# Optimization experiments

Hardware: AMD Instinct MI355X
Metric: run time of the kernel (lower is better)

## Reference

```python
import jax, jax.numpy as jnp
import numpy as np

# Fixed multi-scale geometry implied by the module's hard-coded reshapes
# (48^2=2304, 24^2=576, 12^2=144; Len_q = 576).
SPATIAL = [(48, 48), (24, 24), (12, 12)]
NH, NP, NL = 6, 4, 3  # num_heads, num_points, num_levels


def _process_reference_points(rp):
    """rp: (B, 3024, 2) normalized refs over 3 levels -> (B, 576, 2).
    Mirrors the part1/part2/part3 averaging in MSDeformAttn.forward."""
    B = rp.shape[0]
    p1 = rp[:, :2304].reshape(B, 48, 48, 2).mean(axis=(1, 2))[:, None, :]
    p1 = jnp.broadcast_to(p1, (B, 576, 2))
    p2 = rp[:, 2304:2880].reshape(B, 576, 2)
    p3 = rp[:, 2880:].reshape(B, 12, 12, 2)
    p3 = jax.image.resize(p3, (B, 24, 24, 2), 'bilinear')  # align_corners=False
    p3 = p3.reshape(B, 576, 2)
    return (p1 + p2 + p3) / 3.0


def _bilinear_sample(val_l, coords, Hl, Wl):
    """val_l: (B, Hl*Wl, nh, d) one level's values.
    coords: (B, Lq, nh, P, 2) normalized (x, y) sampling locations.
    Returns (B, Lq, P, nh, d) bilinearly sampled values (zero padding)."""
    B, Lq, nh, P, _ = coords.shape
    px = coords[..., 0] * Wl - 0.5
    py = coords[..., 1] * Hl - 0.5
    x0 = jnp.floor(px)
    y0 = jnp.floor(py)
    lx = px - x0
    ly = py - y0
    x0i = x0.astype(jnp.int32)
    y0i = y0.astype(jnp.int32)

    def _flat(a):  # (B,Lq,nh,P) -> (B,Lq*P,nh,1) matching value layout
        return a.transpose(0, 1, 3, 2).reshape(B, Lq * P, nh, 1)

    def gather(xi, yi):
        valid = (xi >= 0) & (xi < Wl) & (yi >= 0) & (yi < Hl)
        xi_c = jnp.clip(xi, 0, Wl - 1)
        yi_c = jnp.clip(yi, 0, Hl - 1)
        idx = _flat(yi_c * Wl + xi_c)
        v = jnp.take_along_axis(val_l, idx, axis=1)  # (B,Lq*P,nh,d)
        return v * _flat(valid).astype(val_l.dtype)

    w00 = _flat((1 - lx) * (1 - ly))
    w10 = _flat(lx * (1 - ly))
    w01 = _flat((1 - lx) * ly)
    w11 = _flat(lx * ly)
    out = (gather(x0i, y0i) * w00 + gather(x0i + 1, y0i) * w10 +
           gather(x0i, y0i + 1) * w01 + gather(x0i + 1, y0i + 1) * w11)
    return out.reshape(B, Lq, P, nh, -1)


def setup_inputs() -> dict:
    key = jax.random.key(0)
    ks = jax.random.split(key, 8)
    B, C = 32, 384
    Lq, Lv = 576, 3024
    # reference points exactly as get_reference_points builds them
    refs = []
    for (Hl, Wl) in SPATIAL:
        ry, rx = np.meshgrid(np.linspace(0.5, Hl - 0.5, Hl) / Hl,
                             np.linspace(0.5, Wl - 0.5, Wl) / Wl, indexing='ij')
        refs.append(np.stack([rx.ravel(), ry.ravel()], -1))
    rp = np.concatenate(refs, 0).astype(np.float32)  # (3024, 2)
    rp = np.broadcast_to(rp[None, :, None, :], (B, Lv, 1, 2)).copy()
    s = 1.0 / np.sqrt(C)
    return {
        'query': jax.random.normal(ks[0], (B, Lq, C), jnp.float32),
        'value': jax.random.normal(ks[1], (B, Lv, C), jnp.float32),
        'reference_points': jnp.asarray(rp),
        'W_value': jax.random.normal(ks[2], (C, C), jnp.float32) * s,
        'b_value': jnp.zeros((C,), jnp.float32),
        'W_off': jax.random.normal(ks[3], (C, NH * NL * NP * 2), jnp.float32) * 0.01,
        'b_off': jnp.zeros((NH * NL * NP * 2,), jnp.float32),
        'W_attn': jax.random.normal(ks[4], (C, NH * NL * NP), jnp.float32) * s,
        'b_attn': jnp.zeros((NH * NL * NP,), jnp.float32),
        'W_out': jax.random.normal(ks[5], (C, C), jnp.float32) * s,
        'b_out': jnp.zeros((C,), jnp.float32),
    }


def reference(query, value, reference_points, W_value, b_value, W_off, b_off,
              W_attn, b_attn, W_out, b_out):
    B, Lq, C = query.shape
    d = C // NH
    val = (value @ W_value + b_value).reshape(B, -1, NH, d)
    off = (query @ W_off + b_off).reshape(B, Lq, NH, NL, NP, 2)
    attn = jax.nn.softmax((query @ W_attn + b_attn)
                          .reshape(B, Lq, NH, NL * NP), axis=-1)
    attn = attn.reshape(B, Lq, NH, NL, NP)
    ref = _process_reference_points(reference_points.reshape(B, -1, 2))
    coords = off + ref[:, :, None, None, None, :]  # (B,Lq,nh,L,P,2)
    out = jnp.zeros((B, Lq, NH, d), query.dtype)
    start = 0
    for l, (Hl, Wl) in enumerate(SPATIAL):
        val_l = val[:, start:start + Hl * Wl]
        sampled = _bilinear_sample(val_l, coords[:, :, :, l], Hl, Wl)
        out = out + jnp.einsum('bqpnd,bqnp->bqnd', sampled, attn[:, :, :, l])
        start += Hl * Wl
    return out.reshape(B, Lq, NH * d) @ W_out + b_out
```

## Files before the change

kernel.cpp:

```cpp
#include <hip/hip_runtime.h>
#include <cmath>

#define B_SZ   32
#define LQ     576
#define LV     3024
#define CDIM   384
#define NHEAD  6
#define DHEAD  64
#define NLVL   3
#define NPTS   4
#define NPROJ  216
#define NPROJP 256

typedef short    bx4 __attribute__((ext_vector_type(4)));
typedef short    bx8 __attribute__((ext_vector_type(8)));
typedef float    fx4 __attribute__((ext_vector_type(4)));
typedef _Float16 hx8 __attribute__((ext_vector_type(8)));

__device__ __forceinline__ short f2bf(float f) {
    unsigned u = __builtin_bit_cast(unsigned, f);
    unsigned r = (u + 0x7FFFu + ((u >> 16) & 1u)) >> 16;
    return (short)r;
}
__device__ __forceinline__ float bf2f(unsigned short u) {
    return __builtin_bit_cast(float, ((unsigned)u) << 16);
}
__device__ __forceinline__ short f2h(float f) {
    return __builtin_bit_cast(short, (_Float16)f);
}

__global__ __launch_bounds__(256) void cast_bf16_kernel(
    const float4* __restrict__ in, bx8* __restrict__ outv, int n8)
{
    const int i = blockIdx.x * 256 + threadIdx.x;
    if (i >= n8) return;
    const float4 a = in[2 * i], b = in[2 * i + 1];
    bx8 s;
    s[0] = f2bf(a.x); s[1] = f2bf(a.y); s[2] = f2bf(a.z); s[3] = f2bf(a.w);
    s[4] = f2bf(b.x); s[5] = f2bf(b.y); s[6] = f2bf(b.z); s[7] = f2bf(b.w);
    outv[i] = s;
}

__global__ __launch_bounds__(256) void cast_transpose_kernel(
    const float* __restrict__ W, short* __restrict__ Wt, int K, int N)
{
    int idx = blockIdx.x * 256 + threadIdx.x;
    if (idx >= K * N) return;
    int n = idx / K, k = idx - n * K;
    Wt[idx] = f2bf(W[(size_t)k * N + n]);
}

__global__ __launch_bounds__(256) void prep_proj_f16_kernel(
    const float* __restrict__ W_off, const float* __restrict__ b_off,
    const float* __restrict__ W_attn, const float* __restrict__ b_attn,
    short* __restrict__ Wf, float* __restrict__ bc)
{
    int idx = blockIdx.x * 256 + threadIdx.x;
    if (idx >= NPROJP * CDIM) return;
    int n = idx / CDIM, k = idx - n * CDIM;
    float w = 0.f;
    if (n < 144)           w = W_off[(size_t)k * 144 + n];
    else if (n < NPROJ)    w = W_attn[(size_t)k * 72 + (n - 144)];
    Wf[idx] = f2h(w);
    if (idx < NPROJP)
        bc[idx] = (idx < 144) ? b_off[idx]
                 : (idx < NPROJ ? b_attn[idx - 144] : 0.f);
}

template <bool OUT_BF16>
__global__ __launch_bounds__(256) void gemm_dma_kernel(
    const short* __restrict__ A, const short* __restrict__ Bt,
    const float* __restrict__ bias, void* __restrict__ Cout,
    int M, int K)
{
    constexpr int N = 384;
    __shared__ short As[128 * 64];
    __shared__ short Bs[128 * 64];

    const int tid = threadIdx.x;
    const int n0 = blockIdx.x * 128;
    const int m0 = blockIdx.y * 128;

    const int w  = tid >> 6;
    const int l  = tid & 63;
    const int wr = (w & 1) * 64;
    const int wc = (w >> 1) * 64;
    const int lr = l & 15;
    const int q  = l >> 4;

    const int rg  = l >> 3;
    const int cg  = l & 7;
    const int csw = cg ^ rg;

    fx4 acc[4][4] = {};

    for (int k0 = 0; k0 < K; k0 += 64) {
        #pragma unroll
        for (int t = 0; t < 4; ++t) {
            const int rbase = w * 32 + t * 8;
            const short* gA = A + (size_t)(m0 + rbase + rg) * K + k0 + csw * 8;
            __builtin_amdgcn_global_load_lds(
                (const __attribute__((address_space(1))) void*)gA,
                (__attribute__((address_space(3))) void*)&As[rbase * 64],
                16, 0, 0);
            const short* gB = Bt + (size_t)(n0 + rbase + rg) * K + k0 + csw * 8;
            __builtin_amdgcn_global_load_lds(
                (const __attribute__((address_space(1))) void*)gB,
                (__attribute__((address_space(3))) void*)&Bs[rbase * 64],
                16, 0, 0);
        }
        __syncthreads();

        #pragma unroll
        for (int ks = 0; ks < 2; ++ks) {
            bx8 af[4], bf[4];
            #pragma unroll
            for (int i = 0; i < 4; ++i)
                af[i] = *(const bx8*)&As[(wr + i * 16 + lr) * 64 +
                                         (((ks * 4 + q) ^ (lr & 7)) << 3)];
            #pragma unroll
            for (int j = 0; j < 4; ++j)
                bf[j] = *(const bx8*)&Bs[(wc + j * 16 + lr) * 64 +
                                         (((ks * 4 + q) ^ (lr & 7)) << 3)];
            #pragma unroll
            for (int i = 0; i < 4; ++i)
                #pragma unroll
                for (int j = 0; j < 4; ++j)
                    acc[i][j] = __builtin_amdgcn_mfma_f32_16x16x32_bf16(
                        af[i], bf[j], acc[i][j], 0, 0, 0);
        }
        __syncthreads();
    }

    const int rrow = q * 4;
    #pragma unroll
    for (int j = 0; j < 4; ++j) {
        const int col = n0 + wc + j * 16 + lr;
        const float bv = bias[col];
        #pragma unroll
        for (int i = 0; i < 4; ++i) {
            const int row = m0 + wr + i * 16 + rrow;
            #pragma unroll
            for (int r = 0; r < 4; ++r) {
                if (OUT_BF16)
                    ((short*)Cout)[(size_t)(row + r) * N + col] = f2bf(acc[i][j][r] + bv);
                else
                    ((float*)Cout)[(size_t)(row + r) * N + col] = acc[i][j][r] + bv;
            }
        }
    }
}

__global__ __launch_bounds__(256) void gemm_proj_kernel(
    const float* __restrict__ A, const short* __restrict__ Wf,
    const float* __restrict__ bias, float* __restrict__ C,
    int M, int K)
{
    __shared__ short As[128 * 72];
    __shared__ short Bs[128 * 72];

    const int tid = threadIdx.x;
    const int n0 = blockIdx.x * 128;
    const int m0 = blockIdx.y * 128;

    const int w  = tid >> 6;
    const int l  = tid & 63;
    const int wr = (w & 1) * 64;
    const int wc = (w >> 1) * 64;
    const int lr = l & 15;
    const int ko = (l >> 4) * 8;

    fx4 acc[4][4] = {};

    for (int k0 = 0; k0 < K; k0 += 64) {
        #pragma unroll
        for (int r = 0; r < 8; ++r) {
            const int id = tid + r * 256;
            const int m  = id >> 4;
            const int kq = (id & 15) << 2;
            const float4 v = *(const float4*)(A + (size_t)(m0 + m) * K + k0 + kq);
            bx4 s;
            s[0] = f2h(v.x); s[1] = f2h(v.y); s[2] = f2h(v.z); s[3] = f2h(v.w);
            *(bx4*)&As[m * 72 + kq] = s;
        }
        #pragma unroll
        for (int r = 0; r < 4; ++r) {
            const int id = tid + r * 256;
            const int n  = id >> 3;
            const int k8 = (id & 7) << 3;
            *(bx8*)&Bs[n * 72 + k8] = *(const bx8*)(Wf + (size_t)(n0 + n) * K + k0 + k8);
        }
        __syncthreads();

        #pragma unroll
        for (int ks = 0; ks < 2; ++ks) {
            bx8 af[4], bf[4];
            #pragma unroll
            for (int i = 0; i < 4; ++i)
                af[i] = *(const bx8*)&As[(wr + i * 16 + lr) * 72 + ks * 32 + ko];
            #pragma unroll
            for (int j = 0; j < 4; ++j)
                bf[j] = *(const bx8*)&Bs[(wc + j * 16 + lr) * 72 + ks * 32 + ko];
            #pragma unroll
            for (int i = 0; i < 4; ++i)
                #pragma unroll
                for (int j = 0; j < 4; ++j)
                    acc[i][j] = __builtin_amdgcn_mfma_f32_16x16x32_f16(
                        __builtin_bit_cast(hx8, af[i]),
                        __builtin_bit_cast(hx8, bf[j]), acc[i][j], 0, 0, 0);
        }
        __syncthreads();
    }

    const int rrow = (l >> 4) * 4;
    #pragma unroll
    for (int j = 0; j < 4; ++j) {
        const int col = n0 + wc + j * 16 + lr;
        if (col >= NPROJ) continue;
        const float bv = bias[col];
        #pragma unroll
        for (int i = 0; i < 4; ++i) {
            const int row = m0 + wr + i * 16 + rrow;
            #pragma unroll
            for (int r = 0; r < 4; ++r)
                C[(size_t)(row + r) * NPROJ + col] = acc[i][j][r] + bv;
        }
    }
}

__global__ __launch_bounds__(256) void ref_kernel(
    const float* __restrict__ rp, float* __restrict__ refp)
{
    const int b = blockIdx.x;
    const float* r = rp + (size_t)b * LV * 2;
    const int tid = threadIdx.x;

    __shared__ float redx[256], redy[256];
    float sx = 0.f, sy = 0.f;
    for (int i = tid; i < 2304; i += 256) {
        sx += r[2 * i + 0];
        sy += r[2 * i + 1];
    }
    redx[tid] = sx; redy[tid] = sy;
    __syncthreads();
    for (int s = 128; s > 0; s >>= 1) {
        if (tid < s) { redx[tid] += redx[tid + s]; redy[tid] += redy[tid + s]; }
        __syncthreads();
    }
    const float p1x = redx[0] * (1.f / 2304.f);
    const float p1y = redy[0] * (1.f / 2304.f);

    const float* g = r + 2880 * 2;
    for (int q = tid; q < 576; q += 256) {
        const float p2x = r[(2304 + q) * 2 + 0];
        const float p2y = r[(2304 + q) * 2 + 1];
        const int qy = q / 24, qx = q % 24;
        const float syc = fminf(fmaxf(0.5f * qy - 0.25f, 0.f), 11.f);
        const float sxc = fminf(fmaxf(0.5f * qx - 0.25f, 0.f), 11.f);
        int y0 = min((int)syc, 10);
        int x0 = min((int)sxc, 10);
        const float fy = syc - (float)y0, fx = sxc - (float)x0;
        const float v00x = g[(y0 * 12 + x0) * 2 + 0],     v00y = g[(y0 * 12 + x0) * 2 + 1];
        const float v10x = g[(y0 * 12 + x0 + 1) * 2 + 0], v10y = g[(y0 * 12 + x0 + 1) * 2 + 1];
        const float v01x = g[((y0 + 1) * 12 + x0) * 2 + 0],     v01y = g[((y0 + 1) * 12 + x0) * 2 + 1];
        const float v11x = g[((y0 + 1) * 12 + x0 + 1) * 2 + 0], v11y = g[((y0 + 1) * 12 + x0 + 1) * 2 + 1];
        const float p3x = (1.f - fy) * ((1.f - fx) * v00x + fx * v10x)
                        + fy * ((1.f - fx) * v01x + fx * v11x);
        const float p3y = (1.f - fy) * ((1.f - fx) * v00y + fx * v10y)
                        + fy * ((1.f - fx) * v01y + fx * v11y);
        refp[((size_t)b * LQ + q) * 2 + 0] = (p1x + p2x + p3x) * (1.f / 3.f);
        refp[((size_t)b * LQ + q) * 2 + 1] = (p1y + p2y + p3y) * (1.f / 3.f);
    }
}

__global__ __launch_bounds__(192) void sample_kernel(
    const unsigned short* __restrict__ val, const float* __restrict__ proj,
    const float* __restrict__ refp, unsigned* __restrict__ mid)
{
    const int i = blockIdx.x;
    const int g = i & 7;
    const int r = i >> 3;
    const int b = g * 4 + (r / LQ);
    const int q = r - (r / LQ) * LQ;
    const int bq = b * LQ + q;
    const int tid = threadIdx.x;

    __shared__ float attn[72];
    __shared__ int   sloc[72][4];
    __shared__ float swt[72][4];

    if (tid < 72) {
        attn[tid] = proj[(size_t)bq * NPROJ + 144 + tid];

        const int h = tid / 12;
        const int rr = tid % 12;
        const int l = rr >> 2;
        const int p = rr & 3;

        const int HL[3] = {48, 24, 12};
        const int ST[3] = {0, 2304, 2880};
        const int Hl = HL[l], Wl = HL[l], st = ST[l];

        const float rx = refp[bq * 2 + 0];
        const float ry = refp[bq * 2 + 1];
        const int oc = ((h * NLVL + l) * NPTS + p) * 2;
        const float cx = proj[(size_t)bq * NPROJ + oc + 0] + rx;
        const float cy = proj[(size_t)bq * NPROJ + oc + 1] + ry;

        const float px = cx * (float)Wl - 0.5f;
        const float py = cy * (float)Hl - 0.5f;
        const float x0f = floorf(px), y0f = floorf(py);
        const float lx = px - x0f, ly = py - y0f;
        const int x0 = (int)x0f, y0 = (int)y0f;

        #pragma unroll
        for (int k = 0; k < 4; ++k) {
            const int dx = k & 1, dy = k >> 1;
            const int xi = x0 + dx, yi = y0 + dy;
            const bool v = (xi >= 0) && (xi < Wl) && (yi >= 0) && (yi < Hl);
            const int xc = min(max(xi, 0), Wl - 1);
            const int yc = min(max(yi, 0), Hl - 1);
            sloc[tid][k] = st + yc * Wl + xc;
            const float wx = dx ? lx : 1.f - lx;
            const float wy = dy ? ly : 1.f - ly;
            swt[tid][k] = v ? wx * wy : 0.f;
        }
    }
    __syncthreads();

    if (tid < NHEAD) {
        float mx = -1e30f;
        #pragma unroll
        for (int j = 0; j < 12; ++j) mx = fmaxf(mx, attn[tid * 12 + j]);
        float s = 0.f;
        #pragma unroll
        for (int j = 0; j < 12; ++j) {
            const float e = expf(attn[tid * 12 + j] - mx);
            attn[tid * 12 + j] = e;
            s += e;
        }
        const float inv = 1.f / s;
        #pragma unroll
        for (int j = 0; j < 12; ++j) attn[tid * 12 + j] *= inv;
    }
    __syncthreads();

    const int h  = tid >> 5;
    const int c2 = (tid & 31) << 1;
    const unsigned* vp = (const unsigned*)(val + (size_t)b * LV * CDIM + h * DHEAD + c2);
    float acc0 = 0.f, acc1 = 0.f;
    #pragma unroll
    for (int s = 0; s < 12; ++s) {
        const int j = h * 12 + s;
        const float a = attn[j];
        float s0 = 0.f, s1 = 0.f;
        #pragma unroll
        for (int k = 0; k < 4; ++k) {
            const unsigned u = vp[(size_t)sloc[j][k] * (CDIM / 2)];
            const float lo = __builtin_bit_cast(float, u << 16);
            const float hi = __builtin_bit_cast(float, u & 0xFFFF0000u);
            s0 += swt[j][k] * lo;
            s1 += swt[j][k] * hi;
        }
        acc0 += a * s0;
        acc1 += a * s1;
    }
    const unsigned lo = (unsigned)(unsigned short)f2bf(acc0);
    const unsigned hi = (unsigned)(unsigned short)f2bf(acc1);
    mid[((size_t)bq * CDIM + h * DHEAD + c2) >> 1] = lo | (hi << 16);
}

extern "C" void kernel_launch(void* const* d_in, const int* in_sizes, int n_in,
                              void* d_out, int out_size, void* d_ws, size_t ws_size,
                              hipStream_t stream)
{
    (void)in_sizes; (void)n_in; (void)out_size; (void)ws_size;

    const float* query   = (const float*)d_in[0];
    const float* value   = (const float*)d_in[1];
    const float* rp      = (const float*)d_in[2];
    const float* W_value = (const float*)d_in[3];
    const float* b_value = (const float*)d_in[4];
    const float* W_off   = (const float*)d_in[5];
    const float* b_off   = (const float*)d_in[6];
    const float* W_attn  = (const float*)d_in[7];
    const float* b_attn  = (const float*)d_in[8];
    const float* W_out   = (const float*)d_in[9];
    const float* b_out   = (const float*)d_in[10];
    float* out = (float*)d_out;

    char* p = (char*)d_ws;
    auto take = [&](size_t bytes) { char* q = p; p += (bytes + 255) & ~(size_t)255; return q; };
    short* valb = (short*)take((size_t)B_SZ * LV * CDIM * 2);
    short* val  = (short*)take((size_t)B_SZ * LV * CDIM * 2);
    short* mid  = (short*)take((size_t)B_SZ * LQ * CDIM * 2);
    short* Wtv  = (short*)take((size_t)CDIM * CDIM * 2);
    short* Wto  = (short*)take((size_t)CDIM * CDIM * 2);
    short* Wf   = (short*)take((size_t)NPROJP * CDIM * 2);
    float* proj = (float*)take((size_t)B_SZ * LQ * NPROJ * 4);
    float* refp = (float*)take((size_t)B_SZ * LQ * 2 * 4);
    float* bc   = (float*)take((size_t)NPROJP * 4);

    const int Mv = B_SZ * LV;
    const int Mq = B_SZ * LQ;
    const int nv8 = Mv * CDIM / 8;

    cast_transpose_kernel<<<(CDIM * CDIM + 255) / 256, 256, 0, stream>>>(
        W_value, Wtv, CDIM, CDIM);
    cast_transpose_kernel<<<(CDIM * CDIM + 255) / 256, 256, 0, stream>>>(
        W_out, Wto, CDIM, CDIM);
    prep_proj_f16_kernel<<<(NPROJP * CDIM + 255) / 256, 256, 0, stream>>>(
        W_off, b_off, W_attn, b_attn, Wf, bc);
    cast_bf16_kernel<<<(nv8 + 255) / 256, 256, 0, stream>>>(
        (const float4*)value, (bx8*)valb, nv8);

    gemm_dma_kernel<true><<<dim3(3, Mv / 128), 256, 0, stream>>>(
        valb, Wtv, b_value, val, Mv, CDIM);
    gemm_proj_kernel<<<dim3(2, Mq / 128), 256, 0, stream>>>(
        query, Wf, bc, proj, Mq, CDIM);
    ref_kernel<<<B_SZ, 256, 0, stream>>>(rp, refp);
    sample_kernel<<<Mq, 192, 0, stream>>>(
        (const unsigned short*)val, proj, refp, (unsigned*)mid);
    gemm_dma_kernel<false><<<dim3(3, Mq / 128), 256, 0, stream>>>(
        mid, Wto, b_out, out, Mq, CDIM);
}
```

Baseline: 398.6 us.

## Fuse fp32-to-bf16 cast of value into a full-width value projection GEMM

Drops the separate cast pass over the value tensor and the bf16 staging buffer. The new GEMM loads fp32 value rows directly, converts them to bf16 in registers and writes them into swizzled LDS. Each 512-thread block now covers the full N=384 width, so the A tile is read only once rather than three times across column blocks. In exchange the B tile grows to 384x64 in LDS and the per-thread accumulators rise to 24 fragments, which may lower occupancy, and the A loads are now synchronous rather than DMA.

```diff
diff --git a/kernel.cpp b/kernel.cpp
--- a/kernel.cpp
+++ b/kernel.cpp
@@ -29,18 +29,6 @@
     return __builtin_bit_cast(short, (_Float16)f);
 }
 
-__global__ __launch_bounds__(256) void cast_bf16_kernel(
-    const float4* __restrict__ in, bx8* __restrict__ outv, int n8)
-{
-    const int i = blockIdx.x * 256 + threadIdx.x;
-    if (i >= n8) return;
-    const float4 a = in[2 * i], b = in[2 * i + 1];
-    bx8 s;
-    s[0] = f2bf(a.x); s[1] = f2bf(a.y); s[2] = f2bf(a.z); s[3] = f2bf(a.w);
-    s[4] = f2bf(b.x); s[5] = f2bf(b.y); s[6] = f2bf(b.z); s[7] = f2bf(b.w);
-    outv[i] = s;
-}
-
 __global__ __launch_bounds__(256) void cast_transpose_kernel(
     const float* __restrict__ W, short* __restrict__ Wt, int K, int N)
 {
@@ -65,6 +53,99 @@
     if (idx < NPROJP)
         bc[idx] = (idx < 144) ? b_off[idx]
                  : (idx < NPROJ ? b_attn[idx - 144] : 0.f);
+}
+
+__global__ __launch_bounds__(512) void value_gemm_kernel(
+    const float* __restrict__ A, const short* __restrict__ Bt,
+    const float* __restrict__ bias, short* __restrict__ Cout,
+    int M, int K)
+{
+    constexpr int N = 384;
+    __shared__ short As[128 * 64];
+    __shared__ short Bs[384 * 64];
+
+    const int tid = threadIdx.x;
+    const int m0 = blockIdx.x * 128;
+
+    const int w  = tid >> 6;
+    const int l  = tid & 63;
+    const int wr = (w & 1) * 64;
+    const int wc = (w >> 1) * 96;
+    const int lr = l & 15;
+    const int q  = l >> 4;
+
+    const int rg  = l >> 3;
+    const int cg  = l & 7;
+    const int csw = cg ^ rg;
+
+    const int am = tid >> 2;
+    const int ak = (tid & 3) << 4;
+
+    fx4 acc[4][6] = {};
+
+    for (int k0 = 0; k0 < K; k0 += 64) {
+        #pragma unroll
+        for (int t = 0; t < 6; ++t) {
+            const int rbase = w * 48 + t * 8;
+            const short* gB = Bt + (size_t)(rbase + rg) * K + k0 + csw * 8;
+            __builtin_amdgcn_global_load_lds(
+                (const __attribute__((address_space(1))) void*)gB,
+                (__attribute__((address_space(3))) void*)&Bs[rbase * 64],
+                16, 0, 0);
+        }
+        {
+            const float* gA = A + (size_t)(m0 + am) * K + k0 + ak;
+            const float4 v0 = *(const float4*)(gA + 0);
+            const float4 v1 = *(const float4*)(gA + 4);
+            const float4 v2 = *(const float4*)(gA + 8);
+            const float4 v3 = *(const float4*)(gA + 12);
+            bx8 s0, s1;
+            s0[0] = f2bf(v0.x); s0[1] = f2bf(v0.y); s0[2] = f2bf(v0.z); s0[3] = f2bf(v0.w);
+            s0[4] = f2bf(v1.x); s0[5] = f2bf(v1.y); s0[6] = f2bf(v1.z); s0[7] = f2bf(v1.w);
+            s1[0] = f2bf(v2.x); s1[1] = f2bf(v2.y); s1[2] = f2bf(v2.z); s1[3] = f2bf(v2.w);
+            s1[4] = f2bf(v3.x); s1[5] = f2bf(v3.y); s1[6] = f2bf(v3.z); s1[7] = f2bf(v3.w);
+            const int ob = ak >> 3;
+            const int o0 = (ob + 0) ^ (am & 7);
+            const int o1 = (ob + 1) ^ (am & 7);
+            *(bx8*)&As[am * 64 + o0 * 8] = s0;
+            *(bx8*)&As[am * 64 + o1 * 8] = s1;
+        }
+        __syncthreads();
+
+        #pragma unroll
+        for (int ks = 0; ks < 2; ++ks) {
+            bx8 af[4], bf[6];
+            #pragma unroll
+            for (int i = 0; i < 4; ++i)
+                af[i] = *(const bx8*)&As[(wr + i * 16 + lr) * 64 +
+                                         (((ks * 4 + q) ^ (lr & 7)) << 3)];
+            #pragma unroll
+            for (int j = 0; j < 6; ++j)
+                bf[j] = *(const bx8*)&Bs[(wc + j * 16 + lr) * 64 +
+                                         (((ks * 4 + q) ^ (lr & 7)) << 3)];
+            #pragma unroll
+            for (int i = 0; i < 4; ++i)
+                #pragma unroll
+                for (int j = 0; j < 6; ++j)
+                    acc[i][j] = __builtin_amdgcn_mfma_f32_16x16x32_bf16(
+                        af[i], bf[j], acc[i][j], 0, 0, 0);
+        }
+        __syncthreads();
+    }
+
+    const int rrow = q * 4;
+    #pragma unroll
+    for (int j = 0; j < 6; ++j) {
+        const int col = wc + j * 16 + lr;
+        const float bv = bias[col];
+        #pragma unroll
+        for (int i = 0; i < 4; ++i) {
+            const int row = m0 + wr + i * 16 + rrow;
+            #pragma unroll
+            for (int r = 0; r < 4; ++r)
+                Cout[(size_t)(row + r) * N + col] = f2bf(acc[i][j][r] + bv);
+        }
+    }
 }
 
 template <bool OUT_BF16>
@@ -391,7 +472,6 @@
 
     char* p = (char*)d_ws;
     auto take = [&](size_t bytes) { char* q = p; p += (bytes + 255) & ~(size_t)255; return q; };
-    short* valb = (short*)take((size_t)B_SZ * LV * CDIM * 2);
     short* val  = (short*)take((size_t)B_SZ * LV * CDIM * 2);
     short* mid  = (short*)take((size_t)B_SZ * LQ * CDIM * 2);
     short* Wtv  = (short*)take((size_t)CDIM * CDIM * 2);
@@ -403,7 +483,6 @@
 
     const int Mv = B_SZ * LV;
     const int Mq = B_SZ * LQ;
-    const int nv8 = Mv * CDIM / 8;
 
     cast_transpose_kernel<<<(CDIM * CDIM + 255) / 256, 256, 0, stream>>>(
         W_value, Wtv, CDIM, CDIM);
@@ -411,11 +490,9 @@
         W_out, Wto, CDIM, CDIM);
     prep_proj_f16_kernel<<<(NPROJP * CDIM + 255) / 256, 256, 0, stream>>>(
         W_off, b_off, W_attn, b_attn, Wf, bc);
-    cast_bf16_kernel<<<(nv8 + 255) / 256, 256, 0, stream>>>(
-        (const float4*)value, (bx8*)valb, nv8);
-
-    gemm_dma_kernel<true><<<dim3(3, Mv / 128), 256, 0, stream>>>(
-        valb, Wtv, b_value, val, Mv, CDIM);
+
+    value_gemm_kernel<<<Mv / 128, 512, 0, stream>>>(
+        value, Wtv, b_value, val, Mv, CDIM);
     gemm_proj_kernel<<<dim3(2, Mq / 128), 256, 0, stream>>>(
         query, Wf, bc, proj, Mq, CDIM);
     ref_kernel<<<B_SZ, 256, 0, stream>>>(rp, refp);
```

New measurement: 368.3 us. 7.6% less time.
